# Kernel optimization log

Measured on AMD Instinct MI355X. Metric: run time of the kernel, lower is better.

The kernel has to match this reference:

```python
import jax, jax.numpy as jnp
import numpy as np

_INF = 1e9  # large finite 'infinity' for squared distances (max real sq-dist ~ 3*47^2)


def _minplus_last(f):
    """Exact 1D squared Euclidean distance transform along the last axis:
    g[x] = min_j f[j] + (x - j)^2 (brute-force min-plus, fully vectorized)."""
    n = f.shape[-1]
    i = jnp.arange(n)
    d2 = ((i[:, None] - i[None, :]) ** 2).astype(f.dtype)  # (n_out, n_in)
    return jnp.min(f[..., None, :] + d2, axis=-1)


def _edt(src):
    """Exact Euclidean distance to the nearest True voxel of `src` over the last
    3 (spatial) axes. Equivalent to scipy.ndimage.distance_transform_edt(~src)
    (distance to nearest zero of ~src). Separable squared-distance passes."""
    f = jnp.where(src, 0.0, _INF).astype(jnp.float32)
    for ax in (-3, -2, -1):
        f = jnp.moveaxis(_minplus_last(jnp.moveaxis(f, ax, -1)), -1, ax)
    return jnp.sqrt(f)


def _signed_distance_maps(onehot):
    """onehot: (B, C, D, H, W) in {0,1}. Returns SDF = posdis - negdis per (b,c),
    zeroed where the class is absent in that batch element (matches torch code)."""
    pos = onehot.astype(bool)
    stacked = jnp.stack([pos, ~pos], axis=0)          # (2, B, C, D, H, W)
    dists = _edt(stacked)                              # exact EDT for both masks
    posdis, negdis = dists[0], dists[1]
    has_pos = pos.any(axis=(-3, -2, -1))               # (B, C)
    sdf = jnp.where(has_pos[..., None, None, None], posdis - negdis, 0.0)
    return sdf


def setup_inputs() -> dict:
    key = jax.random.key(0)
    k1, k2 = jax.random.split(key)
    B, C, D, H, W = 2, 4, 48, 48, 48
    pred = jax.random.normal(k1, (B, C, D, H, W), dtype=jnp.float32)
    target = jax.random.randint(k2, (B, D, H, W), 0, C, dtype=jnp.int64)
    return {"pred": pred, "target": target}


def reference(pred, target):
    num_classes = pred.shape[1]
    # one-hot encode target: (B, C, D, H, W)
    onehot = (target[:, None] == jnp.arange(num_classes)[None, :, None, None, None])
    onehot = onehot.astype(jnp.float32)
    pred_softmax = jax.nn.softmax(pred, axis=1)
    sdf = _signed_distance_maps(onehot)                # no-grad quantity
    return jnp.mean(jnp.abs(pred_softmax * sdf))
```

## Files before the change

kernel.cpp:

```cpp
#include <hip/hip_runtime.h>
#include <hip/hip_bf16.h>


#define SPATIAL 110592
#define NB 2
#define NC 4
#define NLINE 48
#define SLABP 49

__global__ __launch_bounds__(192) void edt_wh_kernel(const int* __restrict__ target,
                                                     float* __restrict__ F,
                                                     float* __restrict__ out) {
    __shared__ float slab[NLINE * SLABP];
    int blk = blockIdx.x;
    int vol = blk / NLINE, d = blk - vol * NLINE;
    int mask = vol >> 3;
    int b = (vol >> 2) & 1, c = vol & 3;
    int tid = threadIdx.x;
    if (blk == 0 && tid == 0) *out = 0.0f;

    const int* tslab = target + (b * NLINE + d) * (NLINE * NLINE);
    for (int idx = tid; idx < NLINE * NLINE; idx += 192) {
        int h = idx / NLINE, w = idx - h * NLINE;
        bool pos = (tslab[idx] == c);
        bool set = mask ? !pos : pos;
        slab[h * SLABP + w] = set ? 0.0f : 1e9f;
    }
    __syncthreads();

    {
        int h = tid >> 2, cx = (tid & 3) * 12;
        float m[12];
#pragma unroll
        for (int k = 0; k < 12; ++k) m[k] = 1e30f;
        float dj = (float)cx;
        for (int j = 0; j < NLINE; ++j) {
            float fj = slab[h * SLABP + j];
            float aj = fmaf(dj, dj, fj);
#pragma unroll
            for (int k = 0; k < 12; ++k)
                m[k] = fminf(m[k], fmaf((float)(2 * k), dj, aj));
            dj -= 1.0f;
        }
        __syncthreads();
#pragma unroll
        for (int k = 0; k < 12; ++k)
            slab[h * SLABP + cx + k] = m[k] + (float)(k * k);
        __syncthreads();
    }

    {
        int w = tid >> 2, cx = (tid & 3) * 12;
        float m[12];
#pragma unroll
        for (int k = 0; k < 12; ++k) m[k] = 1e30f;
        float dj = (float)cx;
        for (int j = 0; j < NLINE; ++j) {
            float fj = slab[j * SLABP + w];
            float aj = fmaf(dj, dj, fj);
#pragma unroll
            for (int k = 0; k < 12; ++k)
                m[k] = fminf(m[k], fmaf((float)(2 * k), dj, aj));
            dj -= 1.0f;
        }
        __syncthreads();
#pragma unroll
        for (int k = 0; k < 12; ++k)
            slab[(cx + k) * SLABP + w] = m[k] + (float)(k * k);
        __syncthreads();
    }

    float* fvol = F + (long)vol * SPATIAL + (long)d * (NLINE * NLINE);
    for (int idx = tid; idx < NLINE * NLINE; idx += 192) {
        int h = idx / NLINE, w = idx - h * NLINE;
        fvol[idx] = slab[h * SLABP + w];
    }
}

__global__ __launch_bounds__(192) void edt_d_reduce_kernel(const float* __restrict__ pred,
                                                           const float* __restrict__ F,
                                                           float* __restrict__ out) {
    __shared__ float slabP[NLINE * SLABP];
    __shared__ float slabN[NLINE * SLABP];
    int blk = blockIdx.x;
    int half = blk & 1;
    int rest = blk >> 1;
    int bc = rest / NLINE, h = rest - bc * NLINE;
    int b = bc >> 2, c = bc & 3;
    int tid = threadIdx.x;

    const float* fp = F + (long)bc * SPATIAL;
    const float* fn = F + (long)(8 + bc) * SPATIAL;
    for (int idx = tid; idx < NLINE * NLINE; idx += 192) {
        int dd = idx / NLINE, w = idx - dd * NLINE;
        long g = (long)dd * (NLINE * NLINE) + h * NLINE + w;
        slabP[dd * SLABP + w] = fp[g];
        slabN[dd * SLABP + w] = fn[g];
    }
    __syncthreads();

    int w = tid >> 2;
    int cx = half * 24 + (tid & 3) * 6;
    float mP[6], mN[6];
#pragma unroll
    for (int k = 0; k < 6; ++k) { mP[k] = 1e30f; mN[k] = 1e30f; }
    float dj = (float)cx;
    for (int j = 0; j < NLINE; ++j) {
        float fpj = slabP[j * SLABP + w];
        float fnj = slabN[j * SLABP + w];
        float aP = fmaf(dj, dj, fpj);
        float aN = fmaf(dj, dj, fnj);
#pragma unroll
        for (int k = 0; k < 6; ++k) {
            float tk = (float)(2 * k);
            mP[k] = fminf(mP[k], fmaf(tk, dj, aP));
            mN[k] = fminf(mN[k], fmaf(tk, dj, aN));
        }
        dj -= 1.0f;
    }

    float acc = 0.0f;
    long pbase = (long)b * NC * SPATIAL + (long)h * NLINE + w;
#pragma unroll
    for (int k = 0; k < 6; ++k) {
        int d = cx + k;
        float psq = mP[k] + (float)(k * k);
        float nsq = mN[k] + (float)(k * k);
        float sdf = (psq > 1e8f) ? 0.0f : (sqrtf(psq) - sqrtf(nsq));
        long base = pbase + (long)d * (NLINE * NLINE);
        float p0 = pred[base];
        float p1 = pred[base + SPATIAL];
        float p2 = pred[base + 2 * SPATIAL];
        float p3 = pred[base + 3 * SPATIAL];
        float mx = fmaxf(fmaxf(p0, p1), fmaxf(p2, p3));
        float e0 = __expf(p0 - mx), e1 = __expf(p1 - mx);
        float e2 = __expf(p2 - mx), e3 = __expf(p3 - mx);
        float sum = e0 + e1 + e2 + e3;
        float ec = (c == 0) ? e0 : (c == 1) ? e1 : (c == 2) ? e2 : e3;
        acc += (ec / sum) * fabsf(sdf);
    }

#pragma unroll
    for (int o = 32; o > 0; o >>= 1) acc += __shfl_down(acc, o, 64);
    __shared__ float wpart[3];
    int lane = tid & 63, wid = tid >> 6;
    if (lane == 0) wpart[wid] = acc;
    __syncthreads();
    if (tid == 0) {
        float v = wpart[0] + wpart[1] + wpart[2];
        atomicAdd(out, v * (1.0f / (float)(NB * NC * SPATIAL)));
    }
}

extern "C" void kernel_launch(void* const* d_in, const int* in_sizes, int n_in,
                              void* d_out, int out_size, void* d_ws, size_t ws_size,
                              hipStream_t stream) {
    const float* pred = (const float*)d_in[0];
    const int* target = (const int*)d_in[1];
    float* out = (float*)d_out;
    float* F = (float*)d_ws;

    edt_wh_kernel<<<2 * NB * NC * NLINE, 192, 0, stream>>>(target, F, out);
    edt_d_reduce_kernel<<<2 * NB * NC * NLINE, 192, 0, stream>>>(pred, F, out);
}
```

Baseline: 94.38 us.

## Replace brute-force W-axis EDT pass with two-sweep 1D distance scan

The first separable EDT pass on a binary mask becomes a forward and backward scan per row that counts distance to the nearest set voxel and squares it. This replaces the O(n^2) min-plus loop. The target slab is staged in shared memory first. The remaining min-plus loops are unrolled by two to pair fminf operations. The scan runs on only 48 threads per block, which serialises that phase but removes most of the arithmetic.

Result: faster. 91.16 us (-3.4%).

```diff
diff --git a/kernel.cpp b/kernel.cpp
--- a/kernel.cpp
+++ b/kernel.cpp
@@ -12,6 +12,7 @@
                                                      float* __restrict__ F,
                                                      float* __restrict__ out) {
     __shared__ float slab[NLINE * SLABP];
+    __shared__ int tsh[NLINE * NLINE];
     int blk = blockIdx.x;
     int vol = blk / NLINE, d = blk - vol * NLINE;
     int mask = vol >> 3;
@@ -20,34 +21,28 @@
     if (blk == 0 && tid == 0) *out = 0.0f;
 
     const int* tslab = target + (b * NLINE + d) * (NLINE * NLINE);
-    for (int idx = tid; idx < NLINE * NLINE; idx += 192) {
-        int h = idx / NLINE, w = idx - h * NLINE;
-        bool pos = (tslab[idx] == c);
-        bool set = mask ? !pos : pos;
-        slab[h * SLABP + w] = set ? 0.0f : 1e9f;
+    for (int idx = tid; idx < NLINE * NLINE; idx += 192) tsh[idx] = tslab[idx];
+    __syncthreads();
+
+    if (tid < NLINE) {
+        int h = tid;
+        int n = 64;
+        for (int w = 0; w < NLINE; ++w) {
+            int t = tsh[h * NLINE + w];
+            bool set = mask ? (t != c) : (t == c);
+            n = set ? 0 : n + 1;
+            slab[h * SLABP + w] = (float)n;
+        }
+        n = 64;
+        for (int w = NLINE - 1; w >= 0; --w) {
+            int t = tsh[h * NLINE + w];
+            bool set = mask ? (t != c) : (t == c);
+            n = set ? 0 : n + 1;
+            float m = fminf(slab[h * SLABP + w], (float)n);
+            slab[h * SLABP + w] = (m >= 48.0f) ? 1e9f : m * m;
+        }
     }
     __syncthreads();
-
-    {
-        int h = tid >> 2, cx = (tid & 3) * 12;
-        float m[12];
-#pragma unroll
-        for (int k = 0; k < 12; ++k) m[k] = 1e30f;
-        float dj = (float)cx;
-        for (int j = 0; j < NLINE; ++j) {
-            float fj = slab[h * SLABP + j];
-            float aj = fmaf(dj, dj, fj);
-#pragma unroll
-            for (int k = 0; k < 12; ++k)
-                m[k] = fminf(m[k], fmaf((float)(2 * k), dj, aj));
-            dj -= 1.0f;
-        }
-        __syncthreads();
-#pragma unroll
-        for (int k = 0; k < 12; ++k)
-            slab[h * SLABP + cx + k] = m[k] + (float)(k * k);
-        __syncthreads();
-    }
 
     {
         int w = tid >> 2, cx = (tid & 3) * 12;
@@ -55,13 +50,18 @@
 #pragma unroll
         for (int k = 0; k < 12; ++k) m[k] = 1e30f;
         float dj = (float)cx;
-        for (int j = 0; j < NLINE; ++j) {
-            float fj = slab[j * SLABP + w];
-            float aj = fmaf(dj, dj, fj);
+        for (int j = 0; j < NLINE; j += 2) {
+            float f0 = slab[j * SLABP + w];
+            float f1 = slab[(j + 1) * SLABP + w];
+            float a0 = fmaf(dj, dj, f0);
+            float dj1 = dj - 1.0f;
+            float a1 = fmaf(dj1, dj1, f1);
 #pragma unroll
-            for (int k = 0; k < 12; ++k)
-                m[k] = fminf(m[k], fmaf((float)(2 * k), dj, aj));
-            dj -= 1.0f;
+            for (int k = 0; k < 12; ++k) {
+                float tk = (float)(2 * k);
+                m[k] = fminf(fminf(m[k], fmaf(tk, dj, a0)), fmaf(tk, dj1, a1));
+            }
+            dj -= 2.0f;
         }
         __syncthreads();
 #pragma unroll
@@ -72,8 +72,8 @@
 
     float* fvol = F + (long)vol * SPATIAL + (long)d * (NLINE * NLINE);
     for (int idx = tid; idx < NLINE * NLINE; idx += 192) {
-        int h = idx / NLINE, w = idx - h * NLINE;
-        fvol[idx] = slab[h * SLABP + w];
+        int h = idx / NLINE, ww = idx - h * NLINE;
+        fvol[idx] = slab[h * SLABP + ww];
     }
 }
 
@@ -92,10 +92,10 @@
     const float* fp = F + (long)bc * SPATIAL;
     const float* fn = F + (long)(8 + bc) * SPATIAL;
     for (int idx = tid; idx < NLINE * NLINE; idx += 192) {
-        int dd = idx / NLINE, w = idx - dd * NLINE;
-        long g = (long)dd * (NLINE * NLINE) + h * NLINE + w;
-        slabP[dd * SLABP + w] = fp[g];
-        slabN[dd * SLABP + w] = fn[g];
+        int dd = idx / NLINE, ww = idx - dd * NLINE;
+        long g = (long)dd * (NLINE * NLINE) + h * NLINE + ww;
+        slabP[dd * SLABP + ww] = fp[g];
+        slabN[dd * SLABP + ww] = fn[g];
     }
     __syncthreads();
 
@@ -105,18 +105,21 @@
 #pragma unroll
     for (int k = 0; k < 6; ++k) { mP[k] = 1e30f; mN[k] = 1e30f; }
     float dj = (float)cx;
-    for (int j = 0; j < NLINE; ++j) {
-        float fpj = slabP[j * SLABP + w];
-        float fnj = slabN[j * SLABP + w];
-        float aP = fmaf(dj, dj, fpj);
-        float aN = fmaf(dj, dj, fnj);
+    for (int j = 0; j < NLINE; j += 2) {
+        float fp0 = slabP[j * SLABP + w];
+        float fn0 = slabN[j * SLABP + w];
+        float fp1 = slabP[(j + 1) * SLABP + w];
+        float fn1 = slabN[(j + 1) * SLABP + w];
+        float dj1 = dj - 1.0f;
+        float aP0 = fmaf(dj, dj, fp0),  aP1 = fmaf(dj1, dj1, fp1);
+        float aN0 = fmaf(dj, dj, fn0),  aN1 = fmaf(dj1, dj1, fn1);
 #pragma unroll
         for (int k = 0; k < 6; ++k) {
             float tk = (float)(2 * k);
-            mP[k] = fminf(mP[k], fmaf(tk, dj, aP));
-            mN[k] = fminf(mN[k], fmaf(tk, dj, aN));
+            mP[k] = fminf(fminf(mP[k], fmaf(tk, dj, aP0)), fmaf(tk, dj1, aP1));
+            mN[k] = fminf(fminf(mN[k], fmaf(tk, dj, aN0)), fmaf(tk, dj1, aN1));
         }
-        dj -= 1.0f;
+        dj -= 2.0f;
     }
 
     float acc = 0.0f;
```
